# Optimization experiments

Measured on AMD Instinct MI355X. Metric: run time of the kernel, lower is better.

The kernel has to match this reference:

```python
import jax, jax.numpy as jnp
import numpy as np

PATCH = 32          # feature map is PATCH x PATCH, N = PATCH**2 tokens
HEADS = 8
HD = 24             # head_dim (hardcoded in Block -> Cluster3D)
P = 4               # proposal_w = proposal_h = 4 -> 16 cluster centers
EPS_NORM = 1e-12    # F.normalize eps
LN_EPS = 1e-5


def _layernorm(x, g, b):
    m = x.mean(-1, keepdims=True)
    v = ((x - m) ** 2).mean(-1, keepdims=True)
    return (x - m) / jnp.sqrt(v + LN_EPS) * g + b


def _cluster3d(xn, f_w, f_b, v_w, v_b, alpha, beta, proj_w, proj_b):
    # xn: [B, N, D] with tokens laid out row-major over a PATCH x PATCH grid
    B, N, D = xn.shape
    M = P * P
    feat = xn @ f_w.T + f_b   # [B, N, HEADS*HD]  (1x1 conv f)
    val = xn @ v_w.T + v_b    # [B, N, HEADS*HD]  (1x1 conv v)

    def to_heads(t):  # channel layout is (e c): head-major
        return t.reshape(B, N, HEADS, HD).transpose(0, 2, 1, 3).reshape(B * HEADS, N, HD)

    fh = to_heads(feat)       # [Bh, N, HD]
    vh = to_heads(val)

    def pool(t):  # AdaptiveAvgPool to (P, P) over the PATCH x PATCH grid
        g = t.reshape(-1, P, PATCH // P, P, PATCH // P, HD).mean(axis=(2, 4))
        return g.reshape(-1, M, HD)

    centers = pool(fh)        # [Bh, M, HD]
    vcenters = pool(vh)       # [Bh, M, HD]

    cn = centers / jnp.clip(jnp.linalg.norm(centers, axis=-1, keepdims=True), EPS_NORM)
    fn = fh / jnp.clip(jnp.linalg.norm(fh, axis=-1, keepdims=True), EPS_NORM)
    sim = beta + alpha * jnp.einsum('bmc,bnc->bmn', cn, fn)   # [Bh, M, N]
    sim = jnp.where(sim >= 0, sim, 0.2 * sim)                 # LeakyReLU(0.2); dropout eval=identity

    # hard top-1 assignment of each token to its best center
    idx = jnp.argmax(sim, axis=1)                              # [Bh, N]
    mask = jax.nn.one_hot(idx, M, dtype=sim.dtype).transpose(0, 2, 1)  # [Bh, M, N]
    mask = jax.lax.stop_gradient(mask)
    sim = sim * mask

    # aggregate tokens into centers, then dispatch back
    agg = (jnp.einsum('bmn,bnc->bmc', sim, vh) + vcenters) / (mask.sum(-1, keepdims=True) + 1.0)
    out = jnp.einsum('bmn,bmc->bnc', sim, agg)                 # [Bh, N, HD]

    out = out.reshape(B, HEADS, N, HD).transpose(0, 2, 1, 3).reshape(B, N, HEADS * HD)
    return out @ proj_w.T + proj_b                             # [B, N, D]


def setup_inputs() -> dict:
    key = jax.random.key(0)
    ks = jax.random.split(key, 8)
    B, N, D, HID, HH = 64, PATCH * PATCH, 512, 2048, HEADS * HD
    s = 0.02
    return {
        'x': jax.random.normal(ks[0], (B, N, D), jnp.float32),
        'ln1_g': jnp.ones((D,), jnp.float32),
        'ln1_b': jnp.zeros((D,), jnp.float32),
        'f_w': jax.random.normal(ks[1], (HH, D), jnp.float32) * s,
        'f_b': jnp.zeros((HH,), jnp.float32),
        'v_w': jax.random.normal(ks[2], (HH, D), jnp.float32) * s,
        'v_b': jnp.zeros((HH,), jnp.float32),
        'sim_alpha': jnp.ones((1,), jnp.float32),
        'sim_beta': jnp.zeros((1,), jnp.float32),
        'proj_w': jax.random.normal(ks[3], (D, HH), jnp.float32) * s,
        'proj_b': jnp.zeros((D,), jnp.float32),
        'ln2_g': jnp.ones((D,), jnp.float32),
        'ln2_b': jnp.zeros((D,), jnp.float32),
        'fc1_w': jax.random.normal(ks[4], (HID, D), jnp.float32) * s,
        'fc1_b': jnp.zeros((HID,), jnp.float32),
        'fc2_w': jax.random.normal(ks[5], (D, HID), jnp.float32) * s,
        'fc2_b': jnp.zeros((D,), jnp.float32),
    }


def reference(x, ln1_g, ln1_b, f_w, f_b, v_w, v_b, sim_alpha, sim_beta,
              proj_w, proj_b, ln2_g, ln2_b, fc1_w, fc1_b, fc2_w, fc2_b):
    x = x + _cluster3d(_layernorm(x, ln1_g, ln1_b), f_w, f_b, v_w, v_b,
                       sim_alpha, sim_beta, proj_w, proj_b)
    h = _layernorm(x, ln2_g, ln2_b)
    h = jax.nn.gelu(h @ fc1_w.T + fc1_b, approximate=False)
    x = x + (h @ fc2_w.T + fc2_b)
    return x
```

## Files before the change

### kernel.cpp

```cpp
#include <hip/hip_runtime.h>


typedef __attribute__((ext_vector_type(8))) short short8;
typedef __attribute__((ext_vector_type(4))) short short4v;
typedef __attribute__((ext_vector_type(4))) float floatx4;

static __device__ __forceinline__ short f2bf(float f) {
  union { float f; unsigned u; } a; a.f = f;
  unsigned r = a.u + 0x7fffu + ((a.u >> 16) & 1u);
  return (short)(r >> 16);
}

static __device__ __forceinline__ void gload_lds16(const short* g, short* l) {
  __builtin_amdgcn_global_load_lds(
      (const __attribute__((address_space(1))) void*)g,
      (__attribute__((address_space(3))) void*)l, 16, 0, 0);
}

__global__ __launch_bounds__(256) void cvt_f32_bf16(
    const float* __restrict__ in, short* __restrict__ out, int n4)
{
  int i = blockIdx.x * 256 + threadIdx.x;
  if (i >= n4) return;
  float4 v = reinterpret_cast<const float4*>(in)[i];
  short4v o;
  o[0] = f2bf(v.x); o[1] = f2bf(v.y); o[2] = f2bf(v.z); o[3] = f2bf(v.w);
  reinterpret_cast<short4v*>(out)[i] = o;
}

__global__ __launch_bounds__(256) void ln_kernel(
    const float* __restrict__ x, const float* __restrict__ g,
    const float* __restrict__ b, short* __restrict__ out)
{
  const int wave = threadIdx.x >> 6, lane = threadIdx.x & 63;
  const size_t row = (size_t)blockIdx.x * 4 + wave;
  const float* xr = x + row * 512;
  const int c = lane * 8;
  float4 v0 = *reinterpret_cast<const float4*>(xr + c);
  float4 v1 = *reinterpret_cast<const float4*>(xr + c + 4);
  float xs[8] = {v0.x, v0.y, v0.z, v0.w, v1.x, v1.y, v1.z, v1.w};
  float s = 0.f, q = 0.f;
#pragma unroll
  for (int k = 0; k < 8; ++k) { s += xs[k]; q += xs[k] * xs[k]; }
#pragma unroll
  for (int off = 32; off; off >>= 1) {
    s += __shfl_xor(s, off);
    q += __shfl_xor(q, off);
  }
  const float mean = s * (1.0f / 512.0f);
  const float var  = q * (1.0f / 512.0f) - mean * mean;
  const float rstd = rsqrtf(var + 1e-5f);
  short8 o;
#pragma unroll
  for (int k = 0; k < 8; ++k)
    o[k] = f2bf((xs[k] - mean) * rstd * g[c + k] + b[c + k]);
  *reinterpret_cast<short8*>(out + row * 512 + c) = o;
}

template<int BM, int BN, int WM, int WN, int EPI>
__global__ __launch_bounds__(256, 2) void gemm_bt(
    const short* __restrict__ A, const short* __restrict__ W,
    const float* __restrict__ bias, const float* __restrict__ resid,
    float* __restrict__ Cf, short* __restrict__ Cb,
    const int N, const int K)
{
  constexpr int BK = 32;
  constexpr int T  = 256;
  constexpr int AC = (BM * BK / 8) / T;
  constexpr int WC = (BN * BK / 8) / T;
  __shared__ short Al[2][BM * BK];
  __shared__ short Wl[2][BN * BK];
  const int tid  = threadIdx.x;
  const int wave = tid >> 6;
  const int lane = tid & 63;
  constexpr int WCOLS = BN / WN;
  const int wm = (wave / WCOLS) * WM;
  const int wn = (wave % WCOLS) * WN;
  constexpr int MI = WM / 16, NJ = WN / 16;
  const int row0 = blockIdx.x * BM;
  const int col0 = blockIdx.y * BN;
  const int r  = lane & 15;
  const int kc = lane >> 4;

  floatx4 acc[MI][NJ];
#pragma unroll
  for (int i = 0; i < MI; ++i)
#pragma unroll
    for (int j = 0; j < NJ; ++j)
      acc[i][j] = (floatx4){0.f, 0.f, 0.f, 0.f};

  const short* Ab = A + (size_t)row0 * K;
  const short* Wb = W + (size_t)col0 * K;

  const short* aSrc[AC]; int aDst[AC];
#pragma unroll
  for (int u = 0; u < AC; ++u) {
    const int cc = u * T + tid;
    const int rr = cc >> 2, sl = cc & 3;
    const int co = sl ^ ((rr >> 1) & 3);
    aSrc[u] = Ab + (size_t)rr * K + co * 8;
    aDst[u] = cc * 8;
  }
  const short* wSrc[WC]; int wDst[WC];
#pragma unroll
  for (int u = 0; u < WC; ++u) {
    const int cc = u * T + tid;
    const int rr = cc >> 2, sl = cc & 3;
    const int co = sl ^ ((rr >> 1) & 3);
    wSrc[u] = Wb + (size_t)rr * K + co * 8;
    wDst[u] = cc * 8;
  }
  int aOff[MI], wOff[NJ];
#pragma unroll
  for (int i = 0; i < MI; ++i) {
    const int rt = wm + 16 * i + r;
    aOff[i] = rt * BK + ((kc ^ ((rt >> 1) & 3)) << 3);
  }
#pragma unroll
  for (int j = 0; j < NJ; ++j) {
    const int rt = wn + 16 * j + r;
    wOff[j] = rt * BK + ((kc ^ ((rt >> 1) & 3)) << 3);
  }

  auto stage = [&](int buf, int k0) {
#pragma unroll
    for (int u = 0; u < AC; ++u) gload_lds16(aSrc[u] + k0, &Al[buf][aDst[u]]);
#pragma unroll
    for (int u = 0; u < WC; ++u) gload_lds16(wSrc[u] + k0, &Wl[buf][wDst[u]]);
  };

  stage(0, 0);
  __syncthreads();
  int cur = 0;
  for (int k0 = BK; k0 <= K; k0 += BK) {
    if (k0 < K) stage(cur ^ 1, k0);
    short8 af[MI], wfr[NJ];
#pragma unroll
    for (int i = 0; i < MI; ++i)
      af[i] = *reinterpret_cast<const short8*>(&Al[cur][aOff[i]]);
#pragma unroll
    for (int j = 0; j < NJ; ++j)
      wfr[j] = *reinterpret_cast<const short8*>(&Wl[cur][wOff[j]]);
#pragma unroll
    for (int i = 0; i < MI; ++i)
#pragma unroll
      for (int j = 0; j < NJ; ++j)
        acc[i][j] = __builtin_amdgcn_mfma_f32_16x16x32_bf16(
            af[i], wfr[j], acc[i][j], 0, 0, 0);
    __syncthreads();
    cur ^= 1;
  }

#pragma unroll
  for (int i = 0; i < MI; ++i) {
#pragma unroll
    for (int j = 0; j < NJ; ++j) {
      const int col = col0 + wn + 16 * j + r;
      const float bv = bias[col];
#pragma unroll
      for (int t = 0; t < 4; ++t) {
        const int rowi = row0 + wm + 16 * i + (lane >> 4) * 4 + t;
        const size_t offo = (size_t)rowi * N + col;
        float v = acc[i][j][t] + bv;
        if (EPI == 0) {
          Cf[offo] = v;
        } else if (EPI == 1) {
          Cf[offo] = v + resid[offo];
        } else {
          v = 0.5f * v * (1.0f + erff(v * 0.70710678118654752f));
          Cb[offo] = f2bf(v);
        }
      }
    }
  }
}

__global__ __launch_bounds__(384) void pool_kernel(
    const float* __restrict__ feat, const float* __restrict__ val,
    float* __restrict__ cn, float* __restrict__ vcent)
{
  const int bh = blockIdx.x;
  const int b = bh >> 3, h = bh & 7;
  const int t = threadIdx.x;
  const int m = t / 24, c = t % 24;
  const int cy = m >> 2, cx = m & 3;
  const size_t base = (size_t)b * 1024 * 192 + h * 24 + c;
  float sf = 0.f, sv = 0.f;
  for (int dy = 0; dy < 8; ++dy) {
    const int ny = (cy * 8 + dy) * 32 + cx * 8;
    for (int dx = 0; dx < 8; ++dx) {
      const size_t off = base + (size_t)(ny + dx) * 192;
      sf += feat[off];
      sv += val[off];
    }
  }
  sf *= (1.0f / 64.0f); sv *= (1.0f / 64.0f);
  __shared__ float cent[16][24];
  cent[m][c] = sf;
  vcent[(size_t)bh * 384 + t] = sv;
  __syncthreads();
  float nrm = 0.f;
#pragma unroll
  for (int k = 0; k < 24; ++k) nrm += cent[m][k] * cent[m][k];
  nrm = fmaxf(sqrtf(nrm), 1e-12f);
  cn[(size_t)bh * 384 + t] = sf / nrm;
}

__global__ __launch_bounds__(256) void sim_kernel(
    const float* __restrict__ feat, const float* __restrict__ cn,
    const float* __restrict__ alpha_p, const float* __restrict__ beta_p,
    float* __restrict__ sval, int* __restrict__ sidx)
{
  const int bh = blockIdx.y;
  const int b = bh >> 3, h = bh & 7;
  __shared__ float cs[384];
  for (int i = threadIdx.x; i < 384; i += 256) cs[i] = cn[(size_t)bh * 384 + i];
  __syncthreads();
  const int n = blockIdx.x * 256 + threadIdx.x;
  const float* f = feat + (size_t)(b * 1024 + n) * 192 + h * 24;
  float v[24];
#pragma unroll
  for (int k = 0; k < 24; k += 4) {
    float4 t4 = *reinterpret_cast<const float4*>(f + k);
    v[k] = t4.x; v[k + 1] = t4.y; v[k + 2] = t4.z; v[k + 3] = t4.w;
  }
  float q = 0.f;
#pragma unroll
  for (int k = 0; k < 24; ++k) q += v[k] * v[k];
  const float inv = 1.0f / fmaxf(sqrtf(q), 1e-12f);
  const float alpha = alpha_p[0], beta = beta_p[0];
  float best = -3.4e38f; int bi = 0;
#pragma unroll
  for (int m = 0; m < 16; ++m) {
    float d = 0.f;
#pragma unroll
    for (int k = 0; k < 24; ++k) d += cs[m * 24 + k] * v[k];
    float s = beta + alpha * (d * inv);
    s = (s < 0.f) ? 0.2f * s : s;
    if (s > best) { best = s; bi = m; }
  }
  sval[(size_t)bh * 1024 + n] = best;
  sidx[(size_t)bh * 1024 + n] = bi;
}

__global__ __launch_bounds__(256) void agg_kernel(
    const float* __restrict__ val, const float* __restrict__ vcent,
    const float* __restrict__ sval, const int* __restrict__ sidx,
    float* __restrict__ agg)
{
  const int bh = blockIdx.x;
  const int b = bh >> 3, h = bh & 7;
  __shared__ float acc[384];
  __shared__ float cnt[16];
  for (int i = threadIdx.x; i < 384; i += 256) acc[i] = 0.f;
  if (threadIdx.x < 16) cnt[threadIdx.x] = 0.f;
  __syncthreads();
  for (int n = threadIdx.x; n < 1024; n += 256) {
    const float s = sval[(size_t)bh * 1024 + n];
    const int m = sidx[(size_t)bh * 1024 + n];
    atomicAdd(&cnt[m], 1.0f);
    const float* vv = val + (size_t)(b * 1024 + n) * 192 + h * 24;
#pragma unroll
    for (int k = 0; k < 24; ++k) atomicAdd(&acc[m * 24 + k], s * vv[k]);
  }
  __syncthreads();
  for (int i = threadIdx.x; i < 384; i += 256) {
    const int m = i / 24;
    agg[(size_t)bh * 384 + i] = (acc[i] + vcent[(size_t)bh * 384 + i]) / (cnt[m] + 1.0f);
  }
}

__global__ __launch_bounds__(256) void dispatch_kernel(
    const float* __restrict__ sval, const int* __restrict__ sidx,
    const float* __restrict__ agg, short* __restrict__ o)
{
  const int g = blockIdx.x * 256 + threadIdx.x;
  const int h = g & 7, n = (g >> 3) & 1023, b = g >> 13;
  const int bh = b * 8 + h;
  const float s = sval[(size_t)bh * 1024 + n];
  const int m = sidx[(size_t)bh * 1024 + n];
  const float* a = agg + (size_t)bh * 384 + m * 24;
  short* op = o + ((size_t)(b * 1024 + n)) * 192 + h * 24;
  short8 pack[3];
#pragma unroll
  for (int k = 0; k < 24; ++k) pack[k >> 3][k & 7] = f2bf(s * a[k]);
  short8* dst = reinterpret_cast<short8*>(op);
  dst[0] = pack[0]; dst[1] = pack[1]; dst[2] = pack[2];
}

extern "C" void kernel_launch(void* const* d_in, const int* in_sizes, int n_in,
                              void* d_out, int out_size, void* d_ws, size_t ws_size,
                              hipStream_t stream)
{
  const float* x      = (const float*)d_in[0];
  const float* ln1_g  = (const float*)d_in[1];
  const float* ln1_b  = (const float*)d_in[2];
  const float* f_w    = (const float*)d_in[3];
  const float* f_b    = (const float*)d_in[4];
  const float* v_w    = (const float*)d_in[5];
  const float* v_b    = (const float*)d_in[6];
  const float* alpha  = (const float*)d_in[7];
  const float* beta   = (const float*)d_in[8];
  const float* proj_w = (const float*)d_in[9];
  const float* proj_b = (const float*)d_in[10];
  const float* ln2_g  = (const float*)d_in[11];
  const float* ln2_b  = (const float*)d_in[12];
  const float* fc1_w  = (const float*)d_in[13];
  const float* fc1_b  = (const float*)d_in[14];
  const float* fc2_w  = (const float*)d_in[15];
  const float* fc2_b  = (const float*)d_in[16];
  float* out = (float*)d_out;

  char* ws = (char*)d_ws;
  size_t off = 0;
  auto alloc = [&](size_t bytes) -> char* {
    char* p = ws + off;
    off = (off + bytes + 255) & ~(size_t)255;
    return p;
  };
  short* xn   = (short*)alloc(67108864);
  float* feat = (float*)alloc(50331648);
  float* val  = (float*)alloc(50331648);
  short* o    = (short*)alloc(25165824);
  float* x1   = (float*)alloc(134217728);
  short* wf   = (short*)alloc(196608);
  short* wv   = (short*)alloc(196608);
  short* wp   = (short*)alloc(196608);
  short* w1   = (short*)alloc(2097152);
  short* w2   = (short*)alloc(2097152);
  float* cnb  = (float*)alloc(786432);
  float* vcb  = (float*)alloc(786432);
  float* agb  = (float*)alloc(786432);
  float* svb  = (float*)alloc(2097152);
  int*   sib  = (int*)  alloc(2097152);
  short* h  = (short*)feat;
  short* h1 = xn;

  cvt_f32_bf16<<<96,   256, 0, stream>>>(f_w,    wf, 24576);
  cvt_f32_bf16<<<96,   256, 0, stream>>>(v_w,    wv, 24576);
  cvt_f32_bf16<<<96,   256, 0, stream>>>(proj_w, wp, 24576);
  cvt_f32_bf16<<<1024, 256, 0, stream>>>(fc1_w,  w1, 262144);
  cvt_f32_bf16<<<1024, 256, 0, stream>>>(fc2_w,  w2, 262144);

  ln_kernel<<<16384, 256, 0, stream>>>(x, ln1_g, ln1_b, xn);

  gemm_bt<256, 64, 64, 64, 0><<<dim3(256, 3), 256, 0, stream>>>(
      xn, wf, f_b, nullptr, feat, nullptr, 192, 512);
  gemm_bt<256, 64, 64, 64, 0><<<dim3(256, 3), 256, 0, stream>>>(
      xn, wv, v_b, nullptr, val, nullptr, 192, 512);

  pool_kernel<<<512, 384, 0, stream>>>(feat, val, cnb, vcb);
  sim_kernel<<<dim3(4, 512), 256, 0, stream>>>(feat, cnb, alpha, beta, svb, sib);
  agg_kernel<<<512, 256, 0, stream>>>(val, vcb, svb, sib, agb);
  dispatch_kernel<<<2048, 256, 0, stream>>>(svb, sib, agb, o);

  gemm_bt<128, 128, 64, 64, 1><<<dim3(512, 4), 256, 0, stream>>>(
      o, wp, proj_b, x, x1, nullptr, 512, 192);

  ln_kernel<<<16384, 256, 0, stream>>>(x1, ln2_g, ln2_b, h);

  for (int c = 0; c < 4; ++c) {
    const short* hA = h + (size_t)c * 16384 * 512;
    gemm_bt<128, 128, 64, 64, 2><<<dim3(128, 16), 256, 0, stream>>>(
        hA, w1, fc1_b, nullptr, nullptr, h1, 2048, 512);
    gemm_bt<128, 64, 64, 32, 1><<<dim3(128, 8), 256, 0, stream>>>(
        h1, w2, fc2_b, x1 + (size_t)c * 16384 * 512,
        out + (size_t)c * 16384 * 512, nullptr, 512, 2048);
  }
  (void)in_sizes; (void)n_in; (void)out_size; (void)ws_size;
}
```

Before: 1.002 ms.

## Triple-buffer GEMM LDS pipeline with vmcnt waits and retune MLP chunking

The GEMM main loop moves from double buffering to a three-stage LDS ring prefetched with global_load_lds. Explicit s_waitcnt vmcnt plus raw s_barrier replace the full __syncthreads, so more loads stay in flight while MFMAs run. Tile shapes for the f/v projections and fc2 change, and when the workspace is large enough the MLP gets a dedicated h1 buffer and runs in 2 chunks instead of 4. This raises LDS use per block, which may limit occupancy, and depends on the hand-counted vmcnt values being correct.

New measurement: 1.099 ms. +9.6%, slower.

```diff
diff --git a/kernel.cpp b/kernel.cpp
--- a/kernel.cpp
+++ b/kernel.cpp
@@ -15,6 +15,15 @@
   __builtin_amdgcn_global_load_lds(
       (const __attribute__((address_space(1))) void*)g,
       (__attribute__((address_space(3))) void*)l, 16, 0, 0);
+}
+
+template<int N> static __device__ __forceinline__ void wait_vmcnt() {
+  static_assert(N == 4 || N == 6 || N == 8 || N == 10 || N == 12, "add case");
+  if constexpr (N == 4)       asm volatile("s_waitcnt vmcnt(4)"  ::: "memory");
+  else if constexpr (N == 6)  asm volatile("s_waitcnt vmcnt(6)"  ::: "memory");
+  else if constexpr (N == 8)  asm volatile("s_waitcnt vmcnt(8)"  ::: "memory");
+  else if constexpr (N == 10) asm volatile("s_waitcnt vmcnt(10)" ::: "memory");
+  else if constexpr (N == 12) asm volatile("s_waitcnt vmcnt(12)" ::: "memory");
 }
 
 __global__ __launch_bounds__(256) void cvt_f32_bf16(
@@ -68,8 +77,9 @@
   constexpr int T  = 256;
   constexpr int AC = (BM * BK / 8) / T;
   constexpr int WC = (BN * BK / 8) / T;
-  __shared__ short Al[2][BM * BK];
-  __shared__ short Wl[2][BN * BK];
+  constexpr int S  = AC + WC;
+  __shared__ short Al[3][BM * BK];
+  __shared__ short Wl[3][BN * BK];
   const int tid  = threadIdx.x;
   const int wave = tid >> 6;
   const int lane = tid & 63;
@@ -129,11 +139,14 @@
     for (int u = 0; u < WC; ++u) gload_lds16(wSrc[u] + k0, &Wl[buf][wDst[u]]);
   };
 
+  const int nt = K / BK;
   stage(0, 0);
-  __syncthreads();
+  stage(1, BK);
+  stage(2, 2 * BK);
   int cur = 0;
-  for (int k0 = BK; k0 <= K; k0 += BK) {
-    if (k0 < K) stage(cur ^ 1, k0);
+  for (int t = 0; t < nt; ++t) {
+    wait_vmcnt<2 * S>();
+    __builtin_amdgcn_s_barrier();
     short8 af[MI], wfr[NJ];
 #pragma unroll
     for (int i = 0; i < MI; ++i)
@@ -141,14 +154,17 @@
 #pragma unroll
     for (int j = 0; j < NJ; ++j)
       wfr[j] = *reinterpret_cast<const short8*>(&Wl[cur][wOff[j]]);
+    asm volatile("s_waitcnt lgkmcnt(0)" ::: "memory");
+    __builtin_amdgcn_sched_barrier(0);
 #pragma unroll
     for (int i = 0; i < MI; ++i)
 #pragma unroll
       for (int j = 0; j < NJ; ++j)
         acc[i][j] = __builtin_amdgcn_mfma_f32_16x16x32_bf16(
             af[i], wfr[j], acc[i][j], 0, 0, 0);
-    __syncthreads();
-    cur ^= 1;
+    __builtin_amdgcn_s_barrier();
+    if (t + 3 < nt) stage(cur, (t + 3) * BK);
+    cur = (cur == 2) ? 0 : cur + 1;
   }
 
 #pragma unroll
@@ -334,7 +350,18 @@
   float* svb  = (float*)alloc(2097152);
   int*   sib  = (int*)  alloc(2097152);
   short* h  = (short*)feat;
-  short* h1 = xn;
+
+  const size_t h1_bytes = 134217728;
+  short* h1;
+  int nchunk;
+  if (ws_size >= off + h1_bytes) {
+    h1 = (short*)alloc(h1_bytes);
+    nchunk = 2;
+  } else {
+    h1 = xn;
+    nchunk = 4;
+  }
+  const int MCH = 65536 / nchunk;
 
   cvt_f32_bf16<<<96,   256, 0, stream>>>(f_w,    wf, 24576);
   cvt_f32_bf16<<<96,   256, 0, stream>>>(v_w,    wv, 24576);
@@ -344,9 +371,9 @@
 
   ln_kernel<<<16384, 256, 0, stream>>>(x, ln1_g, ln1_b, xn);
 
-  gemm_bt<256, 64, 64, 64, 0><<<dim3(256, 3), 256, 0, stream>>>(
+  gemm_bt<128, 64, 64, 32, 0><<<dim3(512, 3), 256, 0, stream>>>(
       xn, wf, f_b, nullptr, feat, nullptr, 192, 512);
-  gemm_bt<256, 64, 64, 64, 0><<<dim3(256, 3), 256, 0, stream>>>(
+  gemm_bt<128, 64, 64, 32, 0><<<dim3(512, 3), 256, 0, stream>>>(
       xn, wv, v_b, nullptr, val, nullptr, 192, 512);
 
   pool_kernel<<<512, 384, 0, stream>>>(feat, val, cnb, vcb);
@@ -359,13 +386,13 @@
 
   ln_kernel<<<16384, 256, 0, stream>>>(x1, ln2_g, ln2_b, h);
 
-  for (int c = 0; c < 4; ++c) {
-    const short* hA = h + (size_t)c * 16384 * 512;
-    gemm_bt<128, 128, 64, 64, 2><<<dim3(128, 16), 256, 0, stream>>>(
+  for (int c = 0; c < nchunk; ++c) {
+    const short* hA = h + (size_t)c * MCH * 512;
+    gemm_bt<128, 128, 64, 64, 2><<<dim3(MCH / 128, 16), 256, 0, stream>>>(
         hA, w1, fc1_b, nullptr, nullptr, h1, 2048, 512);
-    gemm_bt<128, 64, 64, 32, 1><<<dim3(128, 8), 256, 0, stream>>>(
-        h1, w2, fc2_b, x1 + (size_t)c * 16384 * 512,
-        out + (size_t)c * 16384 * 512, nullptr, 512, 2048);
-  }
-  (void)in_sizes; (void)n_in; (void)out_size; (void)ws_size;
-}
+    gemm_bt<128, 128, 64, 64, 1><<<dim3(MCH / 128, 4), 256, 0, stream>>>(
+        h1, w2, fc2_b, x1 + (size_t)c * MCH * 512,
+        out + (size_t)c * MCH * 512, nullptr, 512, 2048);
+  }
+  (void)in_sizes; (void)n_in; (void)out_size;
+}
```
